# Kernel tuning notes

Hardware: AMD Instinct MI355X
Metric: run time of the kernel (lower is better)

The kernel has to match this reference:

```python
import jax, jax.numpy as jnp
import numpy as np

H = 128
H1 = H + 1          # 129
FUSE = H1 * H1 * H1 # 2,146,689


def setup_inputs() -> dict:
    key = jax.random.key(0)
    ks = jax.random.split(key, 9)
    B = 64
    v = jax.random.normal(ks[0], (B, H), dtype=jnp.float32)
    a = jax.random.normal(ks[1], (B, H), dtype=jnp.float32)
    t = jax.random.normal(ks[2], (B, H), dtype=jnp.float32)
    # Linear params stored as [in, out]; xavier-ish scaling
    W1 = jax.random.normal(ks[3], (FUSE, H // 2), dtype=jnp.float32) * (1.0 / np.sqrt(FUSE))
    b1 = jnp.zeros((H // 2,), dtype=jnp.float32)
    W2 = jax.random.normal(ks[4], (H // 2, H // 4), dtype=jnp.float32) * (1.0 / np.sqrt(H // 2))
    b2 = jnp.zeros((H // 4,), dtype=jnp.float32)
    W3 = jax.random.normal(ks[5], (H // 4, 1), dtype=jnp.float32) * (1.0 / np.sqrt(H // 4))
    b3 = jnp.zeros((1,), dtype=jnp.float32)
    return {"v": v, "a": a, "t": t, "W1": W1, "b1": b1,
            "W2": W2, "b2": b2, "W3": W3, "b3": b3}


def reference(v, a, t, W1, b1, W2, b2, W3, b3):
    B = a.shape[0]
    one = jnp.ones((B, 1), dtype=a.dtype)
    a_h = jnp.concatenate([one, a], axis=1)  # [B, H+1]
    v_h = jnp.concatenate([one, v], axis=1)
    t_h = jnp.concatenate([one, t], axis=1)
    # triple outer product: fusion[b,i,j,k] = a_h[b,i]*v_h[b,j]*t_h[b,k]
    fusion = jnp.einsum('bi,bj,bk->bijk', a_h, v_h, t_h).reshape(B, -1)  # [B, (H+1)^3]
    # dropout p applied at eval is identity (torch Dropout in eval / p=0)
    y1 = jax.nn.relu(fusion @ W1 + b1)
    y2 = jax.nn.relu(y1 @ W2 + b2)
    return y2 @ W3 + b3  # [B, 1]
```

## Files before the change

kernel.cpp:

```cpp
#include <hip/hip_runtime.h>
#include <hip/hip_bf16.h>

#define H 128
#define H1 129
#define NSLAB (H1 * H1)
#define KP 164
#define NBLK 768
#define NREP 8

typedef __attribute__((ext_vector_type(8))) short short8;
typedef __attribute__((ext_vector_type(4))) float float4v;
typedef __attribute__((ext_vector_type(2))) int int2v;
typedef __attribute__((ext_vector_type(4))) int int4v;

__device__ __forceinline__ unsigned short f2bf_bits(float x) {
    return __builtin_bit_cast(unsigned short, __float2bfloat16(x));
}
__device__ __forceinline__ unsigned packbf(float x, float y) {
    return (unsigned)f2bf_bits(x) | ((unsigned)f2bf_bits(y) << 16);
}

#define BAR_LGKM() do {                                           \
    asm volatile("s_waitcnt lgkmcnt(0)" ::: "memory");            \
    __builtin_amdgcn_s_barrier();                                 \
    asm volatile("" ::: "memory");                                \
} while (0)

__global__ __launch_bounds__(256, 3) void k1_partial(
        const float* __restrict__ v, const float* __restrict__ a,
        const float* __restrict__ t, const float* __restrict__ W1,
        float* __restrict__ acc)
{
    __shared__ short lds[64 * KP];

    const int tid  = threadIdx.x;
    const int wv   = tid >> 6;
    const int lane = tid & 63;
    const int quad = lane >> 4;
    const int l15  = lane & 15;

    for (int idx = tid; idx < 64 * (KP - 130); idx += 256) {
        int n = idx / (KP - 130), k = 130 + idx % (KP - 130);
        lds[n * KP + k] = 0;
    }

    short8 tf[5];
    const int bt = 16 * wv + l15;
    #pragma unroll
    for (int s = 0; s < 5; ++s) {
        #pragma unroll
        for (int j = 0; j < 8; ++j) {
            int k = 32 * s + 8 * quad + j;
            float val = (k == 0) ? 1.0f : ((k <= H) ? t[bt * H + k - 1] : 0.0f);
            tf[s][j] = (short)f2bf_bits(val);
        }
    }

    const float4v vz = {0.f, 0.f, 0.f, 0.f};
    float4v y1acc[4] = {vz, vz, vz, vz};

    const int s0 = (int)(((long long)blockIdx.x * NSLAB) / NBLK);
    const int s1 = (int)(((long long)(blockIdx.x + 1) * NSLAB) / NBLK);

    const int q = tid & 15;
    const int p16 = tid >> 4;
    const int br0 = 16 * wv + quad * 4;

    float4v ra[4], rb[4];
    float lastrow;
    float ahc[4], vhc[4], ahn[4], vhn[4];

    auto ISSUE = [&](const float* Wp) {
        #pragma unroll
        for (int it = 0; it < 4; ++it) {
            int p = it * 16 + p16;
            ra[it] = *reinterpret_cast<const float4v*>(Wp + (2 * p) * 64 + q * 4);
            rb[it] = *reinterpret_cast<const float4v*>(Wp + (2 * p + 1) * 64 + q * 4);
        }
        lastrow = (tid < 64) ? Wp[128 * 64 + tid] : 0.f;
    };

    auto WRITE = [&]() {
        #pragma unroll
        for (int it = 0; it < 4; ++it) {
            int p = it * 16 + p16;
            #pragma unroll
            for (int c = 0; c < 4; ++c) {
                int n = q * 4 + c;
                *reinterpret_cast<unsigned*>(&lds[n * KP + 2 * p]) = packbf(ra[it][c], rb[it][c]);
            }
        }
        if (tid < 64)
            *reinterpret_cast<unsigned*>(&lds[tid * KP + 128]) = packbf(lastrow, 0.f);
    };

    auto LOADAV = [&](int si, int sj, float* ah, float* vh) {
        #pragma unroll
        for (int r = 0; r < 4; ++r) {
            int br = br0 + r;
            ah[r] = (si == 0) ? 1.0f : a[br * H + si - 1];
            vh[r] = (sj == 0) ? 1.0f : v[br * H + sj - 1];
        }
    };

    auto MFMA_ACC = [&]() {
        float4v D[4] = {vz, vz, vz, vz};
        #pragma unroll
        for (int s = 0; s < 5; ++s) {
            #pragma unroll
            for (int nt = 0; nt < 4; ++nt) {
                int n = nt * 16 + l15;
                int sa = n * KP + 32 * s + 8 * quad;
                int2v lo = *reinterpret_cast<const int2v*>(&lds[sa]);
                int2v hi = *reinterpret_cast<const int2v*>(&lds[sa + 4]);
                int4v w; w.x = lo.x; w.y = lo.y; w.z = hi.x; w.w = hi.y;
                short8 bf = __builtin_bit_cast(short8, w);
                D[nt] = __builtin_amdgcn_mfma_f32_16x16x32_bf16(tf[s], bf, D[nt], 0, 0, 0);
            }
        }
        float4v avv;
        #pragma unroll
        for (int r = 0; r < 4; ++r) avv[r] = ahc[r] * vhc[r];
        #pragma unroll
        for (int nt = 0; nt < 4; ++nt) y1acc[nt] += avv * D[nt];
    };

    int si = s0 / H1, sj = s0 % H1;
    const float* Wb = W1 + (long long)s0 * (H1 * 64);
    ISSUE(Wb);
    LOADAV(si, sj, ahc, vhc);
    int si_n = si, sj_n = sj;

    for (int sl = s0; sl < s1; ++sl) {
        WRITE();
        if (sl + 1 < s1) {
            Wb += H1 * 64;
            ++sj_n; if (sj_n == H1) { sj_n = 0; ++si_n; }
            ISSUE(Wb);
            LOADAV(si_n, sj_n, ahn, vhn);
        }
        BAR_LGKM();
        MFMA_ACC();
        #pragma unroll
        for (int r = 0; r < 4; ++r) { ahc[r] = ahn[r]; vhc[r] = vhn[r]; }
        BAR_LGKM();
    }

    const int rep = blockIdx.x & (NREP - 1);
    float* accr = acc + rep * (64 * 64);
    #pragma unroll
    for (int nt = 0; nt < 4; ++nt) {
        int h = nt * 16 + l15;
        #pragma unroll
        for (int r = 0; r < 4; ++r)
            unsafeAtomicAdd(&accr[(br0 + r) * 64 + h], y1acc[nt][r]);
    }
}

__global__ void k2_tail(const float* __restrict__ acc, const float* __restrict__ b1,
                        const float* __restrict__ W2, const float* __restrict__ b2,
                        const float* __restrict__ W3, const float* __restrict__ b3,
                        float* __restrict__ out)
{
    __shared__ float y1s[64 * 64];
    __shared__ float y2s[64 * 32];
    const int tid = threadIdx.x;

    for (int e = tid; e < 64 * 64; e += 256) {
        float x = b1[e & 63];
        #pragma unroll
        for (int r = 0; r < NREP; ++r) x += acc[r * 64 * 64 + e];
        y1s[e] = x > 0.f ? x : 0.f;
    }
    __syncthreads();
    for (int e = tid; e < 64 * 32; e += 256) {
        int b = e >> 5, h2 = e & 31;
        float s = b2[h2];
        #pragma unroll 8
        for (int h = 0; h < 64; ++h) s += y1s[b * 64 + h] * W2[h * 32 + h2];
        y2s[e] = s > 0.f ? s : 0.f;
    }
    __syncthreads();
    if (tid < 64) {
        float s = b3[0];
        #pragma unroll
        for (int h2 = 0; h2 < 32; ++h2) s += y2s[tid * 32 + h2] * W3[h2];
        out[tid] = s;
    }
}

extern "C" void kernel_launch(void* const* d_in, const int* in_sizes, int n_in,
                              void* d_out, int out_size, void* d_ws, size_t ws_size,
                              hipStream_t stream) {
    const float* v  = (const float*)d_in[0];
    const float* a  = (const float*)d_in[1];
    const float* t  = (const float*)d_in[2];
    const float* W1 = (const float*)d_in[3];
    const float* b1 = (const float*)d_in[4];
    const float* W2 = (const float*)d_in[5];
    const float* b2 = (const float*)d_in[6];
    const float* W3 = (const float*)d_in[7];
    const float* b3 = (const float*)d_in[8];
    float* acc = (float*)d_ws;

    hipMemsetAsync(acc, 0, NREP * 64 * 64 * sizeof(float), stream);
    hipLaunchKernelGGL(k1_partial, dim3(NBLK), dim3(256), 0, stream, v, a, t, W1, acc);
    hipLaunchKernelGGL(k2_tail, dim3(1), dim3(256), 0, stream,
                       acc, b1, W2, b2, W3, b3, (float*)d_out);
}
```

Measured before the change: 728.1 us.

## Double-buffer W1 slab in LDS and widen fragment reads to 128-bit

Splits the shared-memory staging of each W1 slab into two buffers, so the next slab is written while the current one is consumed by MFMA. This removes one of the two barriers per slab iteration. The row pitch grows from 164 to 168 shorts so each B-fragment can be read with one 16-byte LDS load instead of two 8-byte loads. LDS use doubles, which may cut the three-blocks-per-CU occupancy target, and the a/v scale loads now sit on the critical path instead of being prefetched.

```diff
diff --git a/kernel.cpp b/kernel.cpp
--- a/kernel.cpp
+++ b/kernel.cpp
@@ -4,13 +4,12 @@
 #define H 128
 #define H1 129
 #define NSLAB (H1 * H1)
-#define KP 164
+#define KP 168
 #define NBLK 768
 #define NREP 8
 
 typedef __attribute__((ext_vector_type(8))) short short8;
 typedef __attribute__((ext_vector_type(4))) float float4v;
-typedef __attribute__((ext_vector_type(2))) int int2v;
 typedef __attribute__((ext_vector_type(4))) int int4v;
 
 __device__ __forceinline__ unsigned short f2bf_bits(float x) {
@@ -31,7 +30,7 @@
         const float* __restrict__ t, const float* __restrict__ W1,
         float* __restrict__ acc)
 {
-    __shared__ short lds[64 * KP];
+    __shared__ short lds[2][64 * KP];
 
     const int tid  = threadIdx.x;
     const int wv   = tid >> 6;
@@ -39,9 +38,11 @@
     const int quad = lane >> 4;
     const int l15  = lane & 15;
 
-    for (int idx = tid; idx < 64 * (KP - 130); idx += 256) {
-        int n = idx / (KP - 130), k = 130 + idx % (KP - 130);
-        lds[n * KP + k] = 0;
+    for (int idx = tid; idx < 2 * 64 * (KP - 130); idx += 256) {
+        int b = idx / (64 * (KP - 130));
+        int r = idx % (64 * (KP - 130));
+        int n = r / (KP - 130), k = 130 + r % (KP - 130);
+        lds[b][n * KP + k] = 0;
     }
 
     short8 tf[5];
@@ -68,7 +69,6 @@
 
     float4v ra[4], rb[4];
     float lastrow;
-    float ahc[4], vhc[4], ahn[4], vhn[4];
 
     auto ISSUE = [&](const float* Wp) {
         #pragma unroll
@@ -80,70 +80,67 @@
         lastrow = (tid < 64) ? Wp[128 * 64 + tid] : 0.f;
     };
 
-    auto WRITE = [&]() {
+    auto WRITE = [&](int pb) {
+        short* L = lds[pb];
         #pragma unroll
         for (int it = 0; it < 4; ++it) {
             int p = it * 16 + p16;
             #pragma unroll
             for (int c = 0; c < 4; ++c) {
                 int n = q * 4 + c;
-                *reinterpret_cast<unsigned*>(&lds[n * KP + 2 * p]) = packbf(ra[it][c], rb[it][c]);
+                *reinterpret_cast<unsigned*>(&L[n * KP + 2 * p]) = packbf(ra[it][c], rb[it][c]);
             }
         }
         if (tid < 64)
-            *reinterpret_cast<unsigned*>(&lds[tid * KP + 128]) = packbf(lastrow, 0.f);
+            *reinterpret_cast<unsigned*>(&L[tid * KP + 128]) = packbf(lastrow, 0.f);
     };
 
-    auto LOADAV = [&](int si, int sj, float* ah, float* vh) {
+    const float* Wp = W1 + (long long)s0 * (H1 * 64);
+    ISSUE(Wp);
+    int pb = 0;
+    WRITE(pb);
+    Wp += H1 * 64;
+    if (s0 + 1 < s1) ISSUE(Wp);
+    BAR_LGKM();
+
+    int si = s0 / H1, sj = s0 % H1;
+
+    for (int sl = s0; sl < s1; ++sl) {
+        float ah[4], vh[4];
         #pragma unroll
         for (int r = 0; r < 4; ++r) {
             int br = br0 + r;
             ah[r] = (si == 0) ? 1.0f : a[br * H + si - 1];
             vh[r] = (sj == 0) ? 1.0f : v[br * H + sj - 1];
         }
-    };
-
-    auto MFMA_ACC = [&]() {
+
+        const short* L = lds[pb];
         float4v D[4] = {vz, vz, vz, vz};
         #pragma unroll
         for (int s = 0; s < 5; ++s) {
             #pragma unroll
             for (int nt = 0; nt < 4; ++nt) {
                 int n = nt * 16 + l15;
-                int sa = n * KP + 32 * s + 8 * quad;
-                int2v lo = *reinterpret_cast<const int2v*>(&lds[sa]);
-                int2v hi = *reinterpret_cast<const int2v*>(&lds[sa + 4]);
-                int4v w; w.x = lo.x; w.y = lo.y; w.z = hi.x; w.w = hi.y;
+                int4v w = *reinterpret_cast<const int4v*>(&L[n * KP + 32 * s + 8 * quad]);
                 short8 bf = __builtin_bit_cast(short8, w);
                 D[nt] = __builtin_amdgcn_mfma_f32_16x16x32_bf16(tf[s], bf, D[nt], 0, 0, 0);
             }
         }
         float4v avv;
         #pragma unroll
-        for (int r = 0; r < 4; ++r) avv[r] = ahc[r] * vhc[r];
+        for (int r = 0; r < 4; ++r) avv[r] = ah[r] * vh[r];
         #pragma unroll
         for (int nt = 0; nt < 4; ++nt) y1acc[nt] += avv * D[nt];
-    };
-
-    int si = s0 / H1, sj = s0 % H1;
-    const float* Wb = W1 + (long long)s0 * (H1 * 64);
-    ISSUE(Wb);
-    LOADAV(si, sj, ahc, vhc);
-    int si_n = si, sj_n = sj;
-
-    for (int sl = s0; sl < s1; ++sl) {
-        WRITE();
+
         if (sl + 1 < s1) {
-            Wb += H1 * 64;
-            ++sj_n; if (sj_n == H1) { sj_n = 0; ++si_n; }
-            ISSUE(Wb);
-            LOADAV(si_n, sj_n, ahn, vhn);
-        }
-        BAR_LGKM();
-        MFMA_ACC();
-        #pragma unroll
-        for (int r = 0; r < 4; ++r) { ahc[r] = ahn[r]; vhc[r] = vhn[r]; }
-        BAR_LGKM();
+            pb ^= 1;
+            WRITE(pb);
+            Wp += H1 * 64;
+            if (sl + 2 < s1) ISSUE(Wp);
+            BAR_LGKM();
+        }
+
+        ++sj; if (sj == H1) { sj = 0; ++si; }
     }
 
     const int rep = blockIdx.x & (NREP - 1);
```

Result: no change. 729.0 us (+0.1%).
